# Kernel optimization log

Measured on AMD Instinct MI355X. Metric: run time of the kernel, lower is better.

Reference implementation:

```python
import jax, jax.numpy as jnp
import numpy as np

IN_CH = 256
HID = 32
OUT_CH = 32
EPS = 1e-5


def setup_inputs() -> dict:
    key = jax.random.key(0)
    ks = jax.random.split(key, 7)
    B, L = 1, 256
    x = jax.random.normal(ks[0], (B, L, IN_CH), dtype=jnp.float32)
    # nn.Linear(in_channels, hidden_dim)
    W1 = jax.random.normal(ks[1], (IN_CH, HID), dtype=jnp.float32) / np.sqrt(IN_CH)
    b1 = jnp.zeros((HID,), dtype=jnp.float32)
    # nn.LayerNorm(hidden_dim * hidden_dim)
    gamma = jnp.ones((HID * HID,), dtype=jnp.float32)
    beta = jnp.zeros((HID * HID,), dtype=jnp.float32)
    # nn.Linear(hidden_dim * hidden_dim, out_channels)
    W2 = jax.random.normal(ks[2], (HID * HID, OUT_CH), dtype=jnp.float32) / np.sqrt(HID * HID)
    b2 = jnp.zeros((OUT_CH,), dtype=jnp.float32)
    return {"x": x, "W1": W1, "b1": b1, "gamma": gamma, "beta": beta, "W2": W2, "b2": b2}


def reference(x, W1, b1, gamma, beta, W2, b2):
    # a: [B, L, HID]
    a = jnp.einsum('bic,ch->bih', x, W1) + b1
    # outer product: [B, I, J, D, E] -> flatten to [B, I, J, D*E]
    outer = jnp.einsum('bid,bje->bijde', a, a)
    B, I, J, D, E = outer.shape
    outer = outer.reshape(B, I, J, D * E)
    # LayerNorm over last dim
    mu = jnp.mean(outer, axis=-1, keepdims=True)
    var = jnp.mean(jnp.square(outer - mu), axis=-1, keepdims=True)
    normed = (outer - mu) * jax.lax.rsqrt(var + EPS) * gamma + beta
    # final projection: [B, I, J, OUT_CH]
    return jnp.einsum('bijk,ko->bijo', normed, W2) + b2
```

## Files before the change

kernel.cpp:

```cpp
#include <hip/hip_runtime.h>

#define LSEQ 256
#define INC  256
#define HID  32
#define OUTC 32
#define DE   1024
#define EPSV 1e-5f

#define ASTR 260
#define TSTR 36

__global__ __launch_bounds__(256) void k1_a_stats(
    const float* __restrict__ x, const float* __restrict__ W1, const float* __restrict__ b1,
    const float* __restrict__ gamma, const float* __restrict__ beta,
    const float* __restrict__ W2, const float* __restrict__ b2,
    float* __restrict__ a, float* __restrict__ S, float* __restrict__ Q,
    float* __restrict__ GW, float* __restrict__ C)
{
    __shared__ float sh0[256];
    __shared__ float sh1[256];
    __shared__ float shA[128];
    __shared__ float shB[128];
    const int t = threadIdx.x;
    const int b = blockIdx.x;
    if (b < 64) {
        const int r = t >> 6;
        const int h = (t >> 5) & 1;
        const int d = t & 31;
        const int i = b * 4 + r;
        const float* xr = x + i * INC + h * 128;
        const float* w  = W1 + (h * 128) * HID + d;
        float p0 = 0.f, p1 = 0.f;
        #pragma unroll 8
        for (int k = 0; k < 64; ++k) {
            p0 = fmaf(xr[2 * k],     w[(2 * k) * HID],     p0);
            p1 = fmaf(xr[2 * k + 1], w[(2 * k + 1) * HID], p1);
        }
        sh0[t] = p0 + p1;
        __syncthreads();
        if (h == 0) {
            const float tot = sh0[t] + sh0[t + 32] + b1[d];
            a[i * HID + d] = tot;
            shA[r * 32 + d] = tot;
            shB[r * 32 + d] = tot * tot;
        }
        __syncthreads();
        if (t < 4) {
            float s = 0.f, q = 0.f;
            #pragma unroll
            for (int d2 = 0; d2 < 32; ++d2) { s += shA[t * 32 + d2]; q += shB[t * 32 + d2]; }
            S[b * 4 + t] = s;
            Q[b * 4 + t] = q;
        }
    } else {
        const int o = t & 31, chunk = t >> 5;
        float gw = 0.f, bw = 0.f;
        for (int k = 0; k < 128; ++k) {
            const int de = chunk * 128 + k;
            const float w = W2[de * OUTC + o];
            gw = fmaf(gamma[de], w, gw);
            bw = fmaf(beta[de],  w, bw);
        }
        sh0[t] = gw; sh1[t] = bw;
        __syncthreads();
        if (t < 32) {
            float g = 0.f, bb = 0.f;
            #pragma unroll
            for (int c2 = 0; c2 < 8; ++c2) { g += sh0[c2 * 32 + t]; bb += sh1[c2 * 32 + t]; }
            GW[t] = g;
            C[t]  = bb + b2[t];
        }
    }
}

__global__ __launch_bounds__(256) void k2_fused(
    const float* __restrict__ a, const float* __restrict__ S, const float* __restrict__ Q,
    const float* __restrict__ GW, const float* __restrict__ C,
    const float* __restrict__ gamma, const float* __restrict__ W2,
    float* __restrict__ out)
{
    const int j = blockIdx.x, t = threadIdx.x;
    __shared__ float aPad[32 * ASTR];
    __shared__ float tPad[32 * TSTR];
    __shared__ float gL[DE];
    __shared__ float sL[LSEQ];
    __shared__ float qL[LSEQ];
    __shared__ float gwL[OUTC], cL[OUTC];

    {
        const float4* ar4 = (const float4*)(a + t * HID);
        const int base = (t >> 3) * ASTR + (t & 7);
        #pragma unroll
        for (int c = 0; c < 8; ++c) {
            const float4 v = ar4[c];
            const int d = c * 4;
            aPad[base + (d + 0) * 8] = v.x;
            aPad[base + (d + 1) * 8] = v.y;
            aPad[base + (d + 2) * 8] = v.z;
            aPad[base + (d + 3) * 8] = v.w;
        }
    }
    #pragma unroll
    for (int k = t; k < DE; k += 256) gL[k] = gamma[k];
    sL[t] = S[t];
    qL[t] = Q[t];
    if (t < OUTC) { gwL[t] = GW[t]; cL[t] = C[t]; }
    __syncthreads();

    {
        const int d = t >> 3, o0 = (t & 7) * 4;
        const int jb = (j >> 3) * ASTR + (j & 7);
        float4 acc = {0.f, 0.f, 0.f, 0.f};
        #pragma unroll
        for (int e = 0; e < 32; ++e) {
            const float g = gL[d * 32 + e] * aPad[jb + e * 8];
            const float4 w = *(const float4*)(W2 + (d * 32 + e) * OUTC + o0);
            acc.x = fmaf(g, w.x, acc.x);
            acc.y = fmaf(g, w.y, acc.y);
            acc.z = fmaf(g, w.z, acc.z);
            acc.w = fmaf(g, w.w, acc.w);
        }
        *(float4*)(tPad + d * TSTR + o0) = acc;
    }
    __syncthreads();

    const int iT = t >> 3, oT = t & 7;
    const int abase = iT * ASTR;
    float acc[8][4];
    #pragma unroll
    for (int m = 0; m < 8; ++m)
        #pragma unroll
        for (int k = 0; k < 4; ++k) acc[m][k] = 0.f;

    #pragma unroll
    for (int d = 0; d < 32; ++d) {
        const float4 a0 = *(const float4*)(aPad + abase + d * 8);
        const float4 a1 = *(const float4*)(aPad + abase + d * 8 + 4);
        const float4 tf = *(const float4*)(tPad + d * TSTR + oT * 4);
        const float am[8] = {a0.x, a0.y, a0.z, a0.w, a1.x, a1.y, a1.z, a1.w};
        const float tk[4] = {tf.x, tf.y, tf.z, tf.w};
        #pragma unroll
        for (int m = 0; m < 8; ++m)
            #pragma unroll
            for (int k = 0; k < 4; ++k)
                acc[m][k] = fmaf(am[m], tk[k], acc[m][k]);
    }

    const float Sj = sL[j], Qj = qL[j];
    const float gw0 = gwL[oT * 4 + 0], gw1 = gwL[oT * 4 + 1];
    const float gw2 = gwL[oT * 4 + 2], gw3 = gwL[oT * 4 + 3];
    const float c0 = cL[oT * 4 + 0], c1 = cL[oT * 4 + 1];
    const float c2 = cL[oT * 4 + 2], c3 = cL[oT * 4 + 3];

    #pragma unroll
    for (int m = 0; m < 8; ++m) {
        const int i = iT * 8 + m;
        const float Si = sL[i], Qi = qL[i];
        const float mu  = Si * Sj * (1.0f / 1024.0f);
        const float ex2 = Qi * Qj * (1.0f / 1024.0f);
        const float var = ex2 - mu * mu;
        const float r   = rsqrtf(var + EPSV);
        float4 o4;
        o4.x = fmaf(r, acc[m][0] - mu * gw0, c0);
        o4.y = fmaf(r, acc[m][1] - mu * gw1, c1);
        o4.z = fmaf(r, acc[m][2] - mu * gw2, c2);
        o4.w = fmaf(r, acc[m][3] - mu * gw3, c3);
        *(float4*)(out + (i * LSEQ + j) * OUTC + oT * 4) = o4;
    }
}

extern "C" void kernel_launch(void* const* d_in, const int* in_sizes, int n_in,
                              void* d_out, int out_size, void* d_ws, size_t ws_size,
                              hipStream_t stream)
{
    const float* x     = (const float*)d_in[0];
    const float* W1    = (const float*)d_in[1];
    const float* b1    = (const float*)d_in[2];
    const float* gamma = (const float*)d_in[3];
    const float* beta  = (const float*)d_in[4];
    const float* W2    = (const float*)d_in[5];
    const float* b2    = (const float*)d_in[6];
    float* out = (float*)d_out;

    float* ws = (float*)d_ws;
    float* a  = ws;
    float* S  = ws + 8192;
    float* Q  = ws + 8448;
    float* GW = ws + 8704;
    float* C  = ws + 8736;

    k1_a_stats<<<65, 256, 0, stream>>>(x, W1, b1, gamma, beta, W2, b2, a, S, Q, GW, C);
    k2_fused<<<LSEQ, 256, 0, stream>>>(a, S, Q, GW, C, gamma, W2, out);
}
```

Baseline: 80.65 us.

## Fuse stats and main kernels into one cooperative launch with grid sync

Merges the two kernels into a single cooperative kernel. Each of the 256 blocks computes one row of a and its sum and sum-of-squares, block 0 also computes the gamma/beta-weighted W2 reductions, and a grid-wide sync separates this phase from the fused outer-product/LayerNorm/projection phase. This removes one kernel launch and the gap between launches. The gamma shared-memory tile is also padded to avoid bank conflicts. In exchange it depends on cooperative launch and grid-sync overhead, and block 0 does extra serial work that every other block waits on at the barrier.

```diff
diff --git a/kernel.cpp b/kernel.cpp
--- a/kernel.cpp
+++ b/kernel.cpp
@@ -1,4 +1,7 @@
 #include <hip/hip_runtime.h>
+#include <hip/hip_cooperative_groups.h>
+
+namespace cg = cooperative_groups;
 
 #define LSEQ 256
 #define INC  256
@@ -9,86 +12,82 @@
 
 #define ASTR 260
 #define TSTR 36
+#define GSTR 33
 
-__global__ __launch_bounds__(256) void k1_a_stats(
+__global__ __launch_bounds__(256) void fused_all(
     const float* __restrict__ x, const float* __restrict__ W1, const float* __restrict__ b1,
     const float* __restrict__ gamma, const float* __restrict__ beta,
     const float* __restrict__ W2, const float* __restrict__ b2,
-    float* __restrict__ a, float* __restrict__ S, float* __restrict__ Q,
-    float* __restrict__ GW, float* __restrict__ C)
-{
-    __shared__ float sh0[256];
-    __shared__ float sh1[256];
-    __shared__ float shA[128];
-    __shared__ float shB[128];
-    const int t = threadIdx.x;
-    const int b = blockIdx.x;
-    if (b < 64) {
-        const int r = t >> 6;
-        const int h = (t >> 5) & 1;
-        const int d = t & 31;
-        const int i = b * 4 + r;
-        const float* xr = x + i * INC + h * 128;
-        const float* w  = W1 + (h * 128) * HID + d;
-        float p0 = 0.f, p1 = 0.f;
-        #pragma unroll 8
-        for (int k = 0; k < 64; ++k) {
-            p0 = fmaf(xr[2 * k],     w[(2 * k) * HID],     p0);
-            p1 = fmaf(xr[2 * k + 1], w[(2 * k + 1) * HID], p1);
-        }
-        sh0[t] = p0 + p1;
-        __syncthreads();
-        if (h == 0) {
-            const float tot = sh0[t] + sh0[t + 32] + b1[d];
-            a[i * HID + d] = tot;
-            shA[r * 32 + d] = tot;
-            shB[r * 32 + d] = tot * tot;
-        }
-        __syncthreads();
-        if (t < 4) {
-            float s = 0.f, q = 0.f;
-            #pragma unroll
-            for (int d2 = 0; d2 < 32; ++d2) { s += shA[t * 32 + d2]; q += shB[t * 32 + d2]; }
-            S[b * 4 + t] = s;
-            Q[b * 4 + t] = q;
-        }
-    } else {
-        const int o = t & 31, chunk = t >> 5;
-        float gw = 0.f, bw = 0.f;
-        for (int k = 0; k < 128; ++k) {
-            const int de = chunk * 128 + k;
-            const float w = W2[de * OUTC + o];
-            gw = fmaf(gamma[de], w, gw);
-            bw = fmaf(beta[de],  w, bw);
-        }
-        sh0[t] = gw; sh1[t] = bw;
-        __syncthreads();
-        if (t < 32) {
-            float g = 0.f, bb = 0.f;
-            #pragma unroll
-            for (int c2 = 0; c2 < 8; ++c2) { g += sh0[c2 * 32 + t]; bb += sh1[c2 * 32 + t]; }
-            GW[t] = g;
-            C[t]  = bb + b2[t];
-        }
-    }
-}
-
-__global__ __launch_bounds__(256) void k2_fused(
-    const float* __restrict__ a, const float* __restrict__ S, const float* __restrict__ Q,
-    const float* __restrict__ GW, const float* __restrict__ C,
-    const float* __restrict__ gamma, const float* __restrict__ W2,
+    float* __restrict__ aG, float* __restrict__ SG, float* __restrict__ QG,
+    float* __restrict__ GWG, float* __restrict__ CG,
     float* __restrict__ out)
 {
-    const int j = blockIdx.x, t = threadIdx.x;
+    const int b = blockIdx.x, t = threadIdx.x;
+
     __shared__ float aPad[32 * ASTR];
     __shared__ float tPad[32 * TSTR];
-    __shared__ float gL[DE];
+    __shared__ float gLp[32 * GSTR];
     __shared__ float sL[LSEQ];
     __shared__ float qL[LSEQ];
     __shared__ float gwL[OUTC], cL[OUTC];
+    __shared__ float shRed[256];
+    __shared__ float shRed2[256];
+    __shared__ float shRow[HID];
 
     {
-        const float4* ar4 = (const float4*)(a + t * HID);
+        const int d = t & 31, ch = t >> 5;
+        const float* xr = x + b * INC + ch * 32;
+        const float* w  = W1 + (ch * 32) * HID + d;
+        float p = 0.f;
+        #pragma unroll
+        for (int k = 0; k < 32; ++k)
+            p = fmaf(xr[k], w[k * HID], p);
+        shRed[t] = p;
+        __syncthreads();
+        if (t < 32) {
+            float v = b1[t];
+            #pragma unroll
+            for (int c2 = 0; c2 < 8; ++c2) v += shRed[t + 32 * c2];
+            aG[b * HID + t] = v;
+            shRow[t] = v;
+        }
+        __syncthreads();
+        if (t == 0) {
+            float s = 0.f, q = 0.f;
+            #pragma unroll
+            for (int d2 = 0; d2 < 32; ++d2) { s += shRow[d2]; q = fmaf(shRow[d2], shRow[d2], q); }
+            SG[b] = s;
+            QG[b] = q;
+        }
+        if (b == 0) {
+            const int o = t & 31, ck = t >> 5;
+            float gw = 0.f, bw = 0.f;
+            for (int k = 0; k < 128; ++k) {
+                const int de = ck * 128 + k;
+                const float wv = W2[de * OUTC + o];
+                gw = fmaf(gamma[de], wv, gw);
+                bw = fmaf(beta[de],  wv, bw);
+            }
+            __syncthreads();
+            shRed[t] = gw; shRed2[t] = bw;
+            __syncthreads();
+            if (t < 32) {
+                float g = 0.f, bb = 0.f;
+                #pragma unroll
+                for (int c2 = 0; c2 < 8; ++c2) { g += shRed[c2 * 32 + t]; bb += shRed2[c2 * 32 + t]; }
+                GWG[t] = g;
+                CG[t]  = bb + b2[t];
+            }
+        }
+    }
+
+    __threadfence();
+    cg::this_grid().sync();
+
+    const int j = b;
+
+    {
+        const float4* ar4 = (const float4*)(aG + t * HID);
         const int base = (t >> 3) * ASTR + (t & 7);
         #pragma unroll
         for (int c = 0; c < 8; ++c) {
@@ -101,10 +100,10 @@
         }
     }
     #pragma unroll
-    for (int k = t; k < DE; k += 256) gL[k] = gamma[k];
-    sL[t] = S[t];
-    qL[t] = Q[t];
-    if (t < OUTC) { gwL[t] = GW[t]; cL[t] = C[t]; }
+    for (int k = t; k < DE; k += 256) gLp[(k >> 5) * GSTR + (k & 31)] = gamma[k];
+    sL[t] = SG[t];
+    qL[t] = QG[t];
+    if (t < OUTC) { gwL[t] = GWG[t]; cL[t] = CG[t]; }
     __syncthreads();
 
     {
@@ -113,7 +112,7 @@
         float4 acc = {0.f, 0.f, 0.f, 0.f};
         #pragma unroll
         for (int e = 0; e < 32; ++e) {
-            const float g = gL[d * 32 + e] * aPad[jb + e * 8];
+            const float g = gLp[d * GSTR + e] * aPad[jb + e * 8];
             const float4 w = *(const float4*)(W2 + (d * 32 + e) * OUTC + o0);
             acc.x = fmaf(g, w.x, acc.x);
             acc.y = fmaf(g, w.y, acc.y);
@@ -189,6 +188,11 @@
     float* GW = ws + 8704;
     float* C  = ws + 8736;
 
-    k1_a_stats<<<65, 256, 0, stream>>>(x, W1, b1, gamma, beta, W2, b2, a, S, Q, GW, C);
-    k2_fused<<<LSEQ, 256, 0, stream>>>(a, S, Q, GW, C, gamma, W2, out);
+    void* args[] = {
+        (void*)&x, (void*)&W1, (void*)&b1, (void*)&gamma, (void*)&beta,
+        (void*)&W2, (void*)&b2,
+        (void*)&a, (void*)&S, (void*)&Q, (void*)&GW, (void*)&C, (void*)&out
+    };
+    hipLaunchCooperativeKernel((const void*)fused_all, dim3(LSEQ), dim3(256),
+                               args, 0, stream);
 }
```

Measured after the change: 152.8 us. 1.89x slower.
